# Optimization experiments

Measured on AMD Instinct MI355X. Metric: run time of the kernel, lower is better.

Reference implementation:

```python
import jax, jax.numpy as jnp
import numpy as np

EMBED = 1024
HEADS = 16
HEAD_DIM = EMBED // HEADS


def setup_inputs() -> dict:
    key = jax.random.key(0)
    ks = jax.random.split(key, 11)
    B, S, E = 2, 2048, EMBED
    s = 0.02
    return {
        "query": jax.random.normal(ks[0], (B, S, E), jnp.float32),
        "key_": jax.random.normal(ks[1], (B, S, E), jnp.float32),
        "value": jax.random.normal(ks[2], (B, S, E), jnp.float32),
        "Wq": jax.random.normal(ks[3], (E, E), jnp.float32) * s,
        "bq": jnp.zeros((E,), jnp.float32),
        "Wk": jax.random.normal(ks[4], (E, E), jnp.float32) * s,
        "bk": jnp.zeros((E,), jnp.float32),
        "Wv": jax.random.normal(ks[5], (E, E), jnp.float32) * s,
        "bv": jnp.zeros((E,), jnp.float32),
        "Wo": jax.random.normal(ks[6], (E, E), jnp.float32) * s,
        "bo": jnp.zeros((E,), jnp.float32),
    }


def reference(query, key_, value, Wq, bq, Wk, bk, Wv, bv, Wo, bo):
    B, S, E = query.shape
    H, D = HEADS, HEAD_DIM
    # torch Linear: x @ W.T + b, weight stored [out, in]
    Q = (query @ Wq.T + bq).reshape(B, S, H, D).transpose(0, 2, 1, 3)   # [B,H,S,D]
    K = (key_ @ Wk.T + bk).reshape(B, -1, H, D).transpose(0, 2, 1, 3)
    V = (value @ Wv.T + bv).reshape(B, -1, H, D).transpose(0, 2, 1, 3)
    scores = jnp.einsum("bhsd,bhtd->bhst", Q, K) / jnp.sqrt(jnp.float32(D))
    attn_weights = jax.nn.softmax(scores, axis=-1)                      # dropout p=0.0
    attn_out = jnp.einsum("bhst,bhtd->bhsd", attn_weights, V)
    attn_out = attn_out.transpose(0, 2, 1, 3).reshape(B, S, E)
    output = attn_out @ Wo.T + bo
    return output, attn_weights
```

## Files before the change

kernel.cpp:

```cpp
#include <hip/hip_runtime.h>
#include <hip/hip_bf16.h>
#include <cstdint>
#include <cstddef>

#define Bdim 2
#define Sdim 2048
#define Edim 1024
#define Hdim 16
#define Ddim 64
#define KVB 128
#define MROWS (Bdim*Sdim)

typedef __bf16 bf16_t;
typedef __attribute__((ext_vector_type(8))) __bf16 bf16x8;
typedef __attribute__((ext_vector_type(4))) __bf16 bf16x4;
typedef __attribute__((ext_vector_type(4))) float f32x4;

typedef __attribute__((address_space(3))) uint8_t lds8_t;
typedef const __attribute__((address_space(1))) uint8_t glb8_t;

__device__ inline bf16_t f2b(float x) {
    unsigned u = __builtin_bit_cast(unsigned, x);
    unsigned r = u + 0x7fffu + ((u >> 16) & 1u);
    return __builtin_bit_cast(bf16_t, (unsigned short)(r >> 16));
}

__device__ inline void gemm_async(const bf16_t* A, const bf16_t* B, int K,
                                  f32x4 (&acc)[4][4]) {
    __shared__ __align__(16) bf16_t As[128 * 32];
    __shared__ __align__(16) bf16_t Bs[128 * 32];
    const int tid = threadIdx.x;
    const int lane = tid & 63;
    const int w = tid >> 6;
    const int wm = w >> 1, wn = w & 1;
    const int lr = lane & 15, lg = lane >> 4;

    #pragma unroll
    for (int mi = 0; mi < 4; ++mi)
        #pragma unroll
        for (int ni = 0; ni < 4; ++ni)
            acc[mi][ni] = (f32x4){0.f, 0.f, 0.f, 0.f};

    const int srow = (lane >> 2);
    const int scol = (lane & 3) * 8;

    for (int kt = 0; kt < K; kt += 32) {
        __syncthreads();
        #pragma unroll
        for (int i = 0; i < 2; ++i) {
            const int chunk = w * 2 + i;
            const int row = chunk * 16 + srow;
            __builtin_amdgcn_global_load_lds(
                (glb8_t*)(A + (size_t)row * K + kt + scol),
                (lds8_t*)(As + chunk * 512), 16, 0, 0);
            __builtin_amdgcn_global_load_lds(
                (glb8_t*)(B + (size_t)row * K + kt + scol),
                (lds8_t*)(Bs + chunk * 512), 16, 0, 0);
        }
        __syncthreads();
        bf16x8 af[4], bf[4];
        #pragma unroll
        for (int mi = 0; mi < 4; ++mi)
            af[mi] = *(const bf16x8*)&As[(wm * 64 + mi * 16 + lr) * 32 + lg * 8];
        #pragma unroll
        for (int ni = 0; ni < 4; ++ni)
            bf[ni] = *(const bf16x8*)&Bs[(wn * 64 + ni * 16 + lr) * 32 + lg * 8];
        #pragma unroll
        for (int mi = 0; mi < 4; ++mi)
            #pragma unroll
            for (int ni = 0; ni < 4; ++ni)
                acc[mi][ni] = __builtin_amdgcn_mfma_f32_16x16x32_bf16(
                    af[mi], bf[ni], acc[mi][ni], 0, 0, 0);
    }
}

__global__ __launch_bounds__(256) void k_convert(
    const float* __restrict__ Wq, const float* __restrict__ Wk,
    const float* __restrict__ Wv, const float* __restrict__ Wo,
    const float* __restrict__ xq, const float* __restrict__ xk,
    const float* __restrict__ xv,
    bf16_t* __restrict__ Wb, bf16_t* __restrict__ Xb) {
    const int z = blockIdx.y;
    const float* src;
    bf16_t* d;
    float scale = 1.0f;
    if (z < 4) {
        if (blockIdx.x >= 512) return;
        src = (z == 0) ? Wq : (z == 1) ? Wk : (z == 2) ? Wv : Wo;
        scale = (z == 0) ? 0.125f : 1.0f;
        d = Wb + (size_t)z * Edim * Edim;
    } else {
        src = (z == 4) ? xq : (z == 5) ? xk : xv;
        d = Xb + (size_t)(z - 4) * MROWS * Edim;
    }
    const size_t i = (size_t)blockIdx.x * 256 + threadIdx.x;
    const float4* s4 = (const float4*)(src + i * 8);
    float4 a = s4[0], b = s4[1];
    bf16x8 v;
    v[0] = f2b(a.x * scale); v[1] = f2b(a.y * scale);
    v[2] = f2b(a.z * scale); v[3] = f2b(a.w * scale);
    v[4] = f2b(b.x * scale); v[5] = f2b(b.y * scale);
    v[6] = f2b(b.z * scale); v[7] = f2b(b.w * scale);
    *(bf16x8*)(d + i * 8) = v;
}

__global__ __launch_bounds__(256) void k_proj(
    const bf16_t* __restrict__ Xb, const bf16_t* __restrict__ Wb,
    const float* __restrict__ bq, const float* __restrict__ bk, const float* __restrict__ bv,
    bf16_t* __restrict__ Qb, bf16_t* __restrict__ Kswz, bf16_t* __restrict__ Vswz) {
    const int z = blockIdx.z;
    const bf16_t* X = Xb + (size_t)z * MROWS * Edim;
    const bf16_t* W = Wb + (size_t)z * Edim * Edim;
    const float* bias = (z == 0) ? bq : (z == 1) ? bk : bv;
    const float bscale = (z == 0) ? 0.125f : 1.0f;
    const int tm = blockIdx.y, tn = blockIdx.x;
    f32x4 acc[4][4];
    gemm_async(X + (size_t)tm * 128 * Edim, W + (size_t)tn * 128 * Edim, Edim, acc);
    const int tid = threadIdx.x, lane = tid & 63, w = tid >> 6;
    const int wm = w >> 1, wn = w & 1, lr = lane & 15, lg = lane >> 4;
    #pragma unroll
    for (int mi = 0; mi < 4; ++mi)
        #pragma unroll
        for (int ni = 0; ni < 4; ++ni)
            #pragma unroll
            for (int j = 0; j < 4; ++j) {
                int gm = tm * 128 + wm * 64 + mi * 16 + lg * 4 + j;
                int gn = tn * 128 + wn * 64 + ni * 16 + lr;
                float v = acc[mi][ni][j] + bias[gn] * bscale;
                int b = gm >> 11, s = gm & (Sdim - 1);
                int h = gn >> 6, d = gn & (Ddim - 1);
                size_t bh = (size_t)(b * Hdim + h);
                if (z == 0) {
                    Qb[(bh * Sdim + s) * Ddim + d] = f2b(v);
                } else if (z == 1) {
                    size_t idx = ((bh * (Sdim / 16) + (s >> 4)) * 8 + (d >> 3)) * 128
                               + (s & 15) * 8 + (d & 7);
                    Kswz[idx] = f2b(v);
                } else {
                    size_t idx = (((bh * (Sdim / 32) + (s >> 5)) * 4 + (d >> 4)) * 4
                               + ((s >> 3) & 3)) * 128 + (d & 15) * 8 + (s & 7);
                    Vswz[idx] = f2b(v);
                }
            }
}

__global__ __launch_bounds__(256) void k_attn(
    const bf16_t* __restrict__ Qb, const bf16_t* __restrict__ Kswz,
    const bf16_t* __restrict__ Vswz, float* __restrict__ P, bf16_t* __restrict__ AOb) {
    const int wg = blockIdx.x;
    const int id = ((wg & 7) << 7) | (wg >> 3);
    const int bh = id >> 5, qt = id & 31;
    const int b = bh >> 4, h = bh & 15;
    const int tid = threadIdx.x, lane = tid & 63, w = tid >> 6;
    const int lr = lane & 15, lg = lane >> 4;

    __shared__ bf16_t Ps[2][4][16][132];

    const bf16_t* Qp = Qb + ((size_t)bh * Sdim + qt * 64 + w * 16) * Ddim;
    const bf16_t* Kp = Kswz + (size_t)bh * Sdim * Ddim;
    const bf16_t* Vp = Vswz + (size_t)bh * Ddim * Sdim;
    float* Pp = P + (size_t)bh * Sdim * Sdim + (size_t)(qt * 64 + w * 16) * Sdim;

    bf16x8 qf[2];
    #pragma unroll
    for (int kk = 0; kk < 2; ++kk)
        qf[kk] = *(const bf16x8*)(Qp + lr * Ddim + kk * 32 + lg * 8);

    float lsum[4] = {0.f, 0.f, 0.f, 0.f};
    {
        bf16x8 bA[2][2], bB[2][2], bC[2][2];
#define LOADG(buf, g) { \
            _Pragma("unroll") \
            for (int t = 0; t < 2; ++t) { \
                const bf16_t* kp = Kp + (size_t)((g) * 2 + t) * 1024 + lane * 8; \
                buf[t][0] = *(const bf16x8*)(kp); \
                buf[t][1] = *(const bf16x8*)(kp + 512); \
            } }
#define COMPG(buf) { \
            __builtin_amdgcn_s_setprio(1); \
            f32x4 s0 = (f32x4){0.f,0.f,0.f,0.f}, s1 = (f32x4){0.f,0.f,0.f,0.f}; \
            s0 = __builtin_amdgcn_mfma_f32_16x16x32_bf16(qf[0], buf[0][0], s0, 0, 0, 0); \
            s1 = __builtin_amdgcn_mfma_f32_16x16x32_bf16(qf[0], buf[1][0], s1, 0, 0, 0); \
            s0 = __builtin_amdgcn_mfma_f32_16x16x32_bf16(qf[1], buf[0][1], s0, 0, 0, 0); \
            s1 = __builtin_amdgcn_mfma_f32_16x16x32_bf16(qf[1], buf[1][1], s1, 0, 0, 0); \
            __builtin_amdgcn_s_setprio(0); \
            _Pragma("unroll") \
            for (int j = 0; j < 4; ++j) lsum[j] += __expf(s0[j]) + __expf(s1[j]); }
        LOADG(bA, 0); LOADG(bB, 1);
        for (int g = 0; g < 60; g += 3) {
            LOADG(bC, g + 2); COMPG(bA);
            LOADG(bA, g + 3); COMPG(bB);
            LOADG(bB, g + 4); COMPG(bC);
        }
        LOADG(bC, 62); COMPG(bA);
        LOADG(bA, 63); COMPG(bB);
        COMPG(bC); COMPG(bA);
#undef LOADG
#undef COMPG
    }
    #pragma unroll
    for (int mask = 1; mask <= 8; mask <<= 1)
        #pragma unroll
        for (int j = 0; j < 4; ++j)
            lsum[j] += __shfl_xor(lsum[j], mask);
    float il[4];
    #pragma unroll
    for (int j = 0; j < 4; ++j) il[j] = 1.0f / lsum[j];

    f32x4 oacc[4];
    #pragma unroll
    for (int nd = 0; nd < 4; ++nd) oacc[nd] = (f32x4){0.f, 0.f, 0.f, 0.f};

    for (int kt = 0; kt < Sdim / KVB; ++kt) {
        const int cur = kt & 1, prev = cur ^ 1;
        bf16x8 kf[8][2];
        #pragma unroll
        for (int ni = 0; ni < 8; ++ni) {
            const bf16_t* kp = Kp + (size_t)(kt * 8 + ni) * 1024 + lane * 8;
            kf[ni][0] = *(const bf16x8*)(kp);
            kf[ni][1] = *(const bf16x8*)(kp + 512);
        }
        bf16x8 vf[4][4];
        #pragma unroll
        for (int ks = 0; ks < 4; ++ks)
            #pragma unroll
            for (int nd = 0; nd < 4; ++nd)
                vf[ks][nd] = *(const bf16x8*)(Vp + ((size_t)(kt * 4 + ks) * 4 + nd) * 512 + lane * 8);
        if (kt > 0) {
            #pragma unroll
            for (int i = 0; i < 8; ++i) {
                int row = 2 * i + (lane >> 5);
                int col0 = (lane & 31) * 4;
                bf16x4 p4 = *(const bf16x4*)&Ps[prev][w][row][col0];
                f32x4 o;
                o[0] = (float)p4[0]; o[1] = (float)p4[1];
                o[2] = (float)p4[2]; o[3] = (float)p4[3];
                *(f32x4*)&Pp[(size_t)row * Sdim + (kt - 1) * KVB + col0] = o;
            }
        }
        __builtin_amdgcn_s_setprio(1);
        #pragma unroll
        for (int ni = 0; ni < 8; ++ni) {
            f32x4 s = (f32x4){0.f, 0.f, 0.f, 0.f};
            s = __builtin_amdgcn_mfma_f32_16x16x32_bf16(qf[0], kf[ni][0], s, 0, 0, 0);
            s = __builtin_amdgcn_mfma_f32_16x16x32_bf16(qf[1], kf[ni][1], s, 0, 0, 0);
            #pragma unroll
            for (int j = 0; j < 4; ++j)
                Ps[cur][w][lg * 4 + j][ni * 16 + lr] = f2b(__expf(s[j]) * il[j]);
        }
        __builtin_amdgcn_s_setprio(0);
        __builtin_amdgcn_s_setprio(1);
        #pragma unroll
        for (int ks = 0; ks < 4; ++ks) {
            bf16x8 pa = *(const bf16x8*)&Ps[cur][w][lr][ks * 32 + lg * 8];
            #pragma unroll
            for (int nd = 0; nd < 4; ++nd)
                oacc[nd] = __builtin_amdgcn_mfma_f32_16x16x32_bf16(pa, vf[ks][nd], oacc[nd], 0, 0, 0);
        }
        __builtin_amdgcn_s_setprio(0);
    }
    #pragma unroll
    for (int i = 0; i < 8; ++i) {
        int row = 2 * i + (lane >> 5);
        int col0 = (lane & 31) * 4;
        bf16x4 p4 = *(const bf16x4*)&Ps[1][w][row][col0];
        f32x4 o;
        o[0] = (float)p4[0]; o[1] = (float)p4[1];
        o[2] = (float)p4[2]; o[3] = (float)p4[3];
        *(f32x4*)&Pp[(size_t)row * Sdim + (Sdim - KVB) + col0] = o;
    }

    #pragma unroll
    for (int nd = 0; nd < 4; ++nd)
        #pragma unroll
        for (int j = 0; j < 4; ++j) {
            int s = qt * 64 + w * 16 + lg * 4 + j;
            int d = nd * 16 + lr;
            AOb[((size_t)(b * Sdim + s)) * Edim + h * Ddim + d] = f2b(oacc[nd][j]);
        }
}

__global__ __launch_bounds__(256) void k_oproj(
    const bf16_t* __restrict__ AOb, const bf16_t* __restrict__ Wob,
    const float* __restrict__ bo, float* __restrict__ out) {
    f32x4 acc[4][4];
    gemm_async(AOb + (size_t)blockIdx.y * 128 * Edim,
               Wob + (size_t)blockIdx.x * 128 * Edim, Edim, acc);
    const int tid = threadIdx.x, lane = tid & 63, w = tid >> 6;
    const int wm = w >> 1, wn = w & 1, lr = lane & 15, lg = lane >> 4;
    #pragma unroll
    for (int mi = 0; mi < 4; ++mi)
        #pragma unroll
        for (int ni = 0; ni < 4; ++ni)
            #pragma unroll
            for (int j = 0; j < 4; ++j) {
                int gm = blockIdx.y * 128 + wm * 64 + mi * 16 + lg * 4 + j;
                int gn = blockIdx.x * 128 + wn * 64 + ni * 16 + lr;
                out[(size_t)gm * Edim + gn] = acc[mi][ni][j] + bo[gn];
            }
}

extern "C" void kernel_launch(void* const* d_in, const int* in_sizes, int n_in,
                              void* d_out, int out_size, void* d_ws, size_t ws_size,
                              hipStream_t stream) {
    const float* query = (const float*)d_in[0];
    const float* key_  = (const float*)d_in[1];
    const float* value = (const float*)d_in[2];
    const float* Wq = (const float*)d_in[3];
    const float* bq = (const float*)d_in[4];
    const float* Wk = (const float*)d_in[5];
    const float* bk = (const float*)d_in[6];
    const float* Wv = (const float*)d_in[7];
    const float* bv = (const float*)d_in[8];
    const float* Wo = (const float*)d_in[9];
    const float* bo = (const float*)d_in[10];

    float* out = (float*)d_out;
    float* P = out + (size_t)MROWS * Edim;
    const size_t PSZ = (size_t)32 * Sdim * Sdim;

    const size_t WSZ = (size_t)Edim * Edim;
    const size_t HSD = (size_t)Bdim * Hdim * Sdim * Ddim;
    bf16_t* Wb   = (bf16_t*)d_ws;
    bf16_t* Qb   = Wb + 4 * WSZ;
    bf16_t* Kswz = Qb + HSD;
    bf16_t* Vswz = Kswz + HSD;
    bf16_t* AOb  = Vswz + HSD;
    bf16_t* Xb   = (bf16_t*)(P + PSZ - 6 * 1024 * 1024);

    k_convert<<<dim3(2048, 7), 256, 0, stream>>>(Wq, Wk, Wv, Wo, query, key_, value,
                                                 Wb, Xb);
    k_proj<<<dim3(8, 32, 3), 256, 0, stream>>>(Xb, Wb, bq, bk, bv, Qb, Kswz, Vswz);
    k_attn<<<dim3(1024), 256, 0, stream>>>(Qb, Kswz, Vswz, P, AOb);
    k_oproj<<<dim3(8, 32, 1), 256, 0, stream>>>(AOb, Wb + 3 * WSZ, bo, out);
}
```

Measured before the change: 280.7 us.

## Split softmax-denominator pass across waves by key range, reduce via LDS

The first pass, which computes row sums of exp(scores), now works differently. Before, every wave scanned all 2048 keys for its own 16 query rows. Now each of the 4 waves scans a quarter of the keys for all 64 query rows of the block. Partial sums go to a small LDS array and are combined after a barrier. Each K tile is loaded once per block instead of once per wave, which cuts redundant global/L2 K traffic. The cost is more Q registers, an LDS reduction and a block-wide sync.

```diff
diff --git a/kernel.cpp b/kernel.cpp
--- a/kernel.cpp
+++ b/kernel.cpp
@@ -155,57 +155,95 @@
     const int lr = lane & 15, lg = lane >> 4;
 
     __shared__ bf16_t Ps[2][4][16][132];
-
-    const bf16_t* Qp = Qb + ((size_t)bh * Sdim + qt * 64 + w * 16) * Ddim;
+    __shared__ float sum_lds[4][64];
+
+    const bf16_t* Qp0 = Qb + ((size_t)bh * Sdim + qt * 64) * Ddim;
+    const bf16_t* Qp  = Qp0 + (size_t)(w * 16) * Ddim;
     const bf16_t* Kp = Kswz + (size_t)bh * Sdim * Ddim;
     const bf16_t* Vp = Vswz + (size_t)bh * Ddim * Sdim;
     float* Pp = P + (size_t)bh * Sdim * Sdim + (size_t)(qt * 64 + w * 16) * Sdim;
 
-    bf16x8 qf[2];
-    #pragma unroll
-    for (int kk = 0; kk < 2; ++kk)
-        qf[kk] = *(const bf16x8*)(Qp + lr * Ddim + kk * 32 + lg * 8);
-
-    float lsum[4] = {0.f, 0.f, 0.f, 0.f};
     {
+        bf16x8 qf1[4][2];
+        #pragma unroll
+        for (int rg = 0; rg < 4; ++rg)
+            #pragma unroll
+            for (int kk = 0; kk < 2; ++kk)
+                qf1[rg][kk] = *(const bf16x8*)(Qp0 + (rg * 16 + lr) * Ddim + kk * 32 + lg * 8);
+
+        float lsum[4][4];
+        #pragma unroll
+        for (int rg = 0; rg < 4; ++rg)
+            #pragma unroll
+            for (int j = 0; j < 4; ++j) lsum[rg][j] = 0.f;
+
+        const bf16_t* Kw = Kp + (size_t)w * 32 * 1024;
         bf16x8 bA[2][2], bB[2][2], bC[2][2];
 #define LOADG(buf, g) { \
             _Pragma("unroll") \
             for (int t = 0; t < 2; ++t) { \
-                const bf16_t* kp = Kp + (size_t)((g) * 2 + t) * 1024 + lane * 8; \
+                const bf16_t* kp = Kw + (size_t)((g) * 2 + t) * 1024 + lane * 8; \
                 buf[t][0] = *(const bf16x8*)(kp); \
                 buf[t][1] = *(const bf16x8*)(kp + 512); \
             } }
 #define COMPG(buf) { \
+            f32x4 sv[2][4]; \
             __builtin_amdgcn_s_setprio(1); \
-            f32x4 s0 = (f32x4){0.f,0.f,0.f,0.f}, s1 = (f32x4){0.f,0.f,0.f,0.f}; \
-            s0 = __builtin_amdgcn_mfma_f32_16x16x32_bf16(qf[0], buf[0][0], s0, 0, 0, 0); \
-            s1 = __builtin_amdgcn_mfma_f32_16x16x32_bf16(qf[0], buf[1][0], s1, 0, 0, 0); \
-            s0 = __builtin_amdgcn_mfma_f32_16x16x32_bf16(qf[1], buf[0][1], s0, 0, 0, 0); \
-            s1 = __builtin_amdgcn_mfma_f32_16x16x32_bf16(qf[1], buf[1][1], s1, 0, 0, 0); \
+            _Pragma("unroll") \
+            for (int t = 0; t < 2; ++t) \
+                _Pragma("unroll") \
+                for (int rg = 0; rg < 4; ++rg) { \
+                    f32x4 s = (f32x4){0.f, 0.f, 0.f, 0.f}; \
+                    s = __builtin_amdgcn_mfma_f32_16x16x32_bf16(qf1[rg][0], buf[t][0], s, 0, 0, 0); \
+                    s = __builtin_amdgcn_mfma_f32_16x16x32_bf16(qf1[rg][1], buf[t][1], s, 0, 0, 0); \
+                    sv[t][rg] = s; \
+                } \
             __builtin_amdgcn_s_setprio(0); \
             _Pragma("unroll") \
-            for (int j = 0; j < 4; ++j) lsum[j] += __expf(s0[j]) + __expf(s1[j]); }
+            for (int t = 0; t < 2; ++t) \
+                _Pragma("unroll") \
+                for (int rg = 0; rg < 4; ++rg) \
+                    _Pragma("unroll") \
+                    for (int j = 0; j < 4; ++j) \
+                        lsum[rg][j] += __expf(sv[t][rg][j]); }
         LOADG(bA, 0); LOADG(bB, 1);
-        for (int g = 0; g < 60; g += 3) {
+        for (int g = 0; g < 12; g += 3) {
             LOADG(bC, g + 2); COMPG(bA);
             LOADG(bA, g + 3); COMPG(bB);
             LOADG(bB, g + 4); COMPG(bC);
         }
-        LOADG(bC, 62); COMPG(bA);
-        LOADG(bA, 63); COMPG(bB);
+        LOADG(bC, 14); COMPG(bA);
+        LOADG(bA, 15); COMPG(bB);
         COMPG(bC); COMPG(bA);
 #undef LOADG
 #undef COMPG
-    }
-    #pragma unroll
-    for (int mask = 1; mask <= 8; mask <<= 1)
-        #pragma unroll
-        for (int j = 0; j < 4; ++j)
-            lsum[j] += __shfl_xor(lsum[j], mask);
+        #pragma unroll
+        for (int mask = 1; mask <= 8; mask <<= 1)
+            #pragma unroll
+            for (int rg = 0; rg < 4; ++rg)
+                #pragma unroll
+                for (int j = 0; j < 4; ++j)
+                    lsum[rg][j] += __shfl_xor(lsum[rg][j], mask);
+        if (lr == 0)
+            #pragma unroll
+            for (int rg = 0; rg < 4; ++rg)
+                #pragma unroll
+                for (int j = 0; j < 4; ++j)
+                    sum_lds[w][rg * 16 + lg * 4 + j] = lsum[rg][j];
+    }
+    __syncthreads();
     float il[4];
     #pragma unroll
-    for (int j = 0; j < 4; ++j) il[j] = 1.0f / lsum[j];
+    for (int j = 0; j < 4; ++j) {
+        int row = w * 16 + lg * 4 + j;
+        il[j] = 1.0f / (sum_lds[0][row] + sum_lds[1][row] +
+                        sum_lds[2][row] + sum_lds[3][row]);
+    }
+
+    bf16x8 qf[2];
+    #pragma unroll
+    for (int kk = 0; kk < 2; ++kk)
+        qf[kk] = *(const bf16x8*)(Qp + lr * Ddim + kk * 32 + lg * 8);
 
     f32x4 oacc[4];
     #pragma unroll
```

After: 269.5 us, median of 2. 4.0% less time.
